# Optimization experiments

Hardware: AMD Instinct MI355X
Metric: run time of the kernel (lower is better)

The kernel has to match this reference:

```python
import jax, jax.numpy as jnp
import numpy as np

R = 32  # voxel resolution


def setup_inputs() -> dict:
    key = jax.random.key(0)
    k1, k2 = jax.random.split(key)
    B, C, N = 8, 64, 100000
    features = jax.random.normal(k1, (B, C, N), dtype=jnp.float32)
    coords = jax.random.uniform(k2, (B, 3, N), dtype=jnp.float32)  # unit cube [0,1]
    return {"features": features, "coords": coords}


def reference(features, coords):
    # features: [B, C, N], coords: [B, 3, N] in [0, 1]
    B, C, N = features.shape
    norm_coords = jnp.clip(coords * R, 0, R - 1)
    vox_coords = jnp.round(norm_coords).astype(jnp.int32)  # [B, 3, N]

    # flat voxel index per point: x*R^2 + y*R + z, offset per batch
    idx = vox_coords[:, 0] * R * R + vox_coords[:, 1] * R + vox_coords[:, 2]  # [B, N]
    flat_idx = (idx + jnp.arange(B, dtype=jnp.int32)[:, None] * (R ** 3)).reshape(-1)  # [B*N]

    feat = jnp.transpose(features, (0, 2, 1)).reshape(B * N, C)  # [B*N, C]
    sums = jax.ops.segment_sum(feat, flat_idx, num_segments=B * R ** 3)  # [B*R^3, C]
    cnt = jax.ops.segment_sum(jnp.ones((B * N,), features.dtype), flat_idx,
                              num_segments=B * R ** 3)  # [B*R^3]
    avg = sums / jnp.maximum(cnt, 1.0)[:, None]  # average; empty voxels stay 0

    vox_feat = jnp.transpose(avg.reshape(B, R ** 3, C), (0, 2, 1)).reshape(B, C, R, R, R)
    return vox_feat, vox_coords.astype(jnp.int64)
```

## Files before the change

kernel.cpp:

```cpp
#include <hip/hip_runtime.h>

#define RR 32
#define R3 32768
#define BATCH 8
#define CH 64
#define NPTS 100000
#define NPOINTS (BATCH * NPTS)
#define NVOX (BATCH * R3)
#define SCAN_BLOCKS (NVOX / 256)

typedef unsigned int uint32;

__device__ __forceinline__ uint32 f2bf(float f) {
    uint32 u = __float_as_uint(f);
    return (u + 0x7fffu + ((u >> 16) & 1u)) >> 16;
}
__device__ __forceinline__ float bf2f(uint32 h) {
    return __uint_as_float(h << 16);
}

__global__ __launch_bounds__(256) void phase1_count(
    const float* __restrict__ coords,
    uint32* __restrict__ vox,
    uint32* __restrict__ cnt,
    float* __restrict__ out2)
{
    int gid = blockIdx.x * blockDim.x + threadIdx.x;
    if (gid >= NPOINTS) return;
    int b = gid / NPTS;
    int n = gid - b * NPTS;

    const float* cb = coords + (size_t)b * 3 * NPTS + n;
    float fx = fminf(fmaxf(cb[0]        * 32.0f, 0.0f), 31.0f);
    float fy = fminf(fmaxf(cb[NPTS]     * 32.0f, 0.0f), 31.0f);
    float fz = fminf(fmaxf(cb[2 * NPTS] * 32.0f, 0.0f), 31.0f);
    int x = (int)rintf(fx);
    int y = (int)rintf(fy);
    int z = (int)rintf(fz);
    uint32 g = (uint32)(b * R3 + x * (RR * RR) + y * RR + z);

    float* o2 = out2 + (size_t)b * 3 * NPTS + n;
    o2[0]        = (float)x;
    o2[NPTS]     = (float)y;
    o2[2 * NPTS] = (float)z;

    vox[gid] = g;
    atomicAdd(&cnt[g], 1u);
}

__global__ __launch_bounds__(256) void scan_block_sums(
    const uint32* __restrict__ cnt, uint32* __restrict__ bsum)
{
    __shared__ uint32 s[256];
    int t = threadIdx.x;
    s[t] = cnt[blockIdx.x * 256 + t];
    __syncthreads();
    for (int off = 128; off > 0; off >>= 1) {
        if (t < off) s[t] += s[t + off];
        __syncthreads();
    }
    if (t == 0) bsum[blockIdx.x] = s[0];
}

__global__ __launch_bounds__(256) void scan_bsum(uint32* __restrict__ bsum)
{
    __shared__ uint32 s[256];
    int t = threadIdx.x;
    uint32 v0 = bsum[4 * t], v1 = bsum[4 * t + 1], v2 = bsum[4 * t + 2], v3 = bsum[4 * t + 3];
    uint32 tot = v0 + v1 + v2 + v3;
    s[t] = tot;
    __syncthreads();
    for (int off = 1; off < 256; off <<= 1) {
        uint32 x = (t >= off) ? s[t - off] : 0u;
        __syncthreads();
        s[t] += x;
        __syncthreads();
    }
    uint32 excl = s[t] - tot;
    bsum[4 * t]     = excl;
    bsum[4 * t + 1] = excl + v0;
    bsum[4 * t + 2] = excl + v0 + v1;
    bsum[4 * t + 3] = excl + v0 + v1 + v2;
}

__global__ __launch_bounds__(256) void scan_final(
    const uint32* __restrict__ cnt, const uint32* __restrict__ bsum,
    uint32* __restrict__ starts, uint32* __restrict__ cursor)
{
    __shared__ uint32 s[256];
    int t = threadIdx.x;
    int gid = blockIdx.x * 256 + t;
    uint32 v = cnt[gid];
    s[t] = v;
    __syncthreads();
    for (int off = 1; off < 256; off <<= 1) {
        uint32 x = (t >= off) ? s[t - off] : 0u;
        __syncthreads();
        s[t] += x;
        __syncthreads();
    }
    uint32 st = bsum[blockIdx.x] + s[t] - v;
    starts[gid] = st;
    cursor[gid] = st;
}

__global__ __launch_bounds__(256) void phase3_scatter(
    const float* __restrict__ feat,
    const uint32* __restrict__ vox,
    uint32* __restrict__ cursor,
    uint4* __restrict__ sorted)
{
    int gid = blockIdx.x * blockDim.x + threadIdx.x;
    if (gid >= NPOINTS) return;
    int b = gid / NPTS;
    int n = gid - b * NPTS;

    uint32 g = vox[gid];
    uint32 pos = atomicAdd(&cursor[g], 1u);

    const float* frow = feat + (size_t)b * CH * NPTS + n;
    uint4* dst = sorted + (size_t)pos * 8;
#pragma unroll
    for (int j = 0; j < 8; ++j) {
        uint4 w;
        float f0 = frow[(size_t)(8 * j + 0) * NPTS];
        float f1 = frow[(size_t)(8 * j + 1) * NPTS];
        float f2 = frow[(size_t)(8 * j + 2) * NPTS];
        float f3 = frow[(size_t)(8 * j + 3) * NPTS];
        float f4 = frow[(size_t)(8 * j + 4) * NPTS];
        float f5 = frow[(size_t)(8 * j + 5) * NPTS];
        float f6 = frow[(size_t)(8 * j + 6) * NPTS];
        float f7 = frow[(size_t)(8 * j + 7) * NPTS];
        w.x = f2bf(f0) | (f2bf(f1) << 16);
        w.y = f2bf(f2) | (f2bf(f3) << 16);
        w.z = f2bf(f4) | (f2bf(f5) << 16);
        w.w = f2bf(f6) | (f2bf(f7) << 16);
        dst[j] = w;
    }
}

__global__ __launch_bounds__(256) void phase4_reduce(
    const uint32* __restrict__ sorted,
    const uint32* __restrict__ starts,
    float* __restrict__ out1)
{
    __shared__ float tile[64][65];

    int gbase = blockIdx.x * 64;
    int tid = threadIdx.x;
    int wave = tid >> 6, lane = tid & 63;

    if (lane < 32) {
        for (int k = 0; k < 16; ++k) {
            int g = gbase + wave * 16 + k;
            uint32 s = starts[g];
            uint32 e = (g == NVOX - 1) ? (uint32)NPOINTS : starts[g + 1];
            float a0 = 0.0f, a1 = 0.0f;
            for (uint32 p = s; p < e; ++p) {
                uint32 w = sorted[(size_t)p * 32 + lane];
                a0 += bf2f(w & 0xffffu);
                a1 += bf2f(w >> 16);
            }
            uint32 c = e - s;
            float rcp = 1.0f / (float)(c > 1u ? c : 1u);
            int vloc = wave * 16 + k;
            tile[vloc][2 * lane]     = a0 * rcp;
            tile[vloc][2 * lane + 1] = a1 * rcp;
        }
    }
    __syncthreads();

    int b = gbase / R3;
    int v0 = gbase - b * R3;
    int vv = tid & 63;
    int c0 = tid >> 6;
    float* obase = out1 + (size_t)b * CH * R3 + v0 + vv;
#pragma unroll
    for (int jj = 0; jj < 16; ++jj) {
        int c = jj * 4 + c0;
        obase[(size_t)c * R3] = tile[vv][c];
    }
}

__global__ __launch_bounds__(256) void accum_direct(
    const float* __restrict__ feat, const float* __restrict__ coords,
    float* __restrict__ out1, uint32* __restrict__ cnt, float* __restrict__ out2)
{
    int gid = blockIdx.x * blockDim.x + threadIdx.x;
    if (gid >= NPOINTS) return;
    int b = gid / NPTS;
    int n = gid - b * NPTS;
    const float* cb = coords + (size_t)b * 3 * NPTS + n;
    float fx = fminf(fmaxf(cb[0]        * 32.0f, 0.0f), 31.0f);
    float fy = fminf(fmaxf(cb[NPTS]     * 32.0f, 0.0f), 31.0f);
    float fz = fminf(fmaxf(cb[2 * NPTS] * 32.0f, 0.0f), 31.0f);
    int x = (int)rintf(fx), y = (int)rintf(fy), z = (int)rintf(fz);
    int v = x * (RR * RR) + y * RR + z;
    float* o2 = out2 + (size_t)b * 3 * NPTS + n;
    o2[0] = (float)x; o2[NPTS] = (float)y; o2[2 * NPTS] = (float)z;
    atomicAdd(&cnt[b * R3 + v], 1u);
    float* obase = out1 + (size_t)(b * CH) * R3 + v;
    const float* frow = feat + (size_t)(b * CH) * NPTS + n;
#pragma unroll 8
    for (int c = 0; c < CH; ++c)
        unsafeAtomicAdd(&obase[(size_t)c * R3], frow[(size_t)c * NPTS]);
}

__global__ __launch_bounds__(256) void finalize_direct(
    float* __restrict__ out1, const uint32* __restrict__ cnt)
{
    size_t gid = (size_t)blockIdx.x * blockDim.x + threadIdx.x;
    size_t total = (size_t)BATCH * CH * R3;
    if (gid >= total) return;
    int v = (int)(gid & (R3 - 1));
    int b = (int)(gid / ((size_t)CH * R3));
    uint32 ct = cnt[b * R3 + v];
    out1[gid] = out1[gid] / (float)(ct > 1u ? ct : 1u);
}

extern "C" void kernel_launch(void* const* d_in, const int* in_sizes, int n_in,
                              void* d_out, int out_size, void* d_ws, size_t ws_size,
                              hipStream_t stream)
{
    const float* feat   = (const float*)d_in[0];
    const float* coords = (const float*)d_in[1];

    float* out1 = (float*)d_out;
    float* out2 = out1 + (size_t)BATCH * CH * R3;

    const size_t vox_off    = 0;
    const size_t vox_bytes  = (size_t)NPOINTS * 4;
    const size_t cnt_off    = vox_off + ((vox_bytes + 255) & ~255ull);
    const size_t cnt_bytes  = (size_t)NVOX * 4;
    const size_t starts_off = cnt_off + ((cnt_bytes + 255) & ~255ull);
    const size_t cursor_off = starts_off + ((cnt_bytes + 255) & ~255ull);
    const size_t bsum_off   = cursor_off + ((cnt_bytes + 255) & ~255ull);
    const size_t bsum_bytes = (size_t)SCAN_BLOCKS * 4;
    const size_t sort_off   = (bsum_off + bsum_bytes + 255) & ~255ull;
    const size_t sort_bytes = (size_t)NPOINTS * 128;
    const size_t need       = sort_off + sort_bytes;

    const int npt_blocks = (NPOINTS + 255) / 256;

    if (ws_size >= need) {
        char* ws = (char*)d_ws;
        uint32* vox    = (uint32*)(ws + vox_off);
        uint32* cnt    = (uint32*)(ws + cnt_off);
        uint32* starts = (uint32*)(ws + starts_off);
        uint32* cursor = (uint32*)(ws + cursor_off);
        uint32* bsum   = (uint32*)(ws + bsum_off);
        uint32* sorted = (uint32*)(ws + sort_off);

        hipMemsetAsync(cnt, 0, cnt_bytes, stream);
        phase1_count<<<npt_blocks, 256, 0, stream>>>(coords, vox, cnt, out2);
        scan_block_sums<<<SCAN_BLOCKS, 256, 0, stream>>>(cnt, bsum);
        scan_bsum<<<1, 256, 0, stream>>>(bsum);
        scan_final<<<SCAN_BLOCKS, 256, 0, stream>>>(cnt, bsum, starts, cursor);
        phase3_scatter<<<npt_blocks, 256, 0, stream>>>(feat, vox, cursor, (uint4*)sorted);
        phase4_reduce<<<NVOX / 64, 256, 0, stream>>>(sorted, starts, out1);
    } else {
        uint32* cnt = (uint32*)d_ws;
        hipMemsetAsync(out1, 0, (size_t)BATCH * CH * R3 * sizeof(float), stream);
        hipMemsetAsync(d_ws, 0, (size_t)NVOX * 4, stream);
        accum_direct<<<npt_blocks, 256, 0, stream>>>(feat, coords, out1, cnt, out2);
        size_t total = (size_t)BATCH * CH * R3;
        finalize_direct<<<(unsigned)((total + 255) / 256), 256, 0, stream>>>(out1, cnt);
    }
}
```

Before: 499.4 us.

## Replace counting-sort pipeline with per-(batch,channel) LDS atomic histogram accumulation

Drops the scan and sort-by-voxel pipeline (three scan kernels, a scatter into a bf16 sorted buffer, and a segmented reduce). Each block now owns one (batch, channel) pair and accumulates all 100k points into a 32768-float LDS array with shared-memory atomics, then divides by the counts and writes the output with coalesced float4 stores. Voxel indices are stored as 16-bit values to halve that traffic. This removes the bf16 rounding and the large sorted intermediate, but it uses 128KB of LDS per block, which limits occupancy, and it depends on LDS float atomics.

After: 522.9 us. +4.7%, slower.

```diff
diff --git a/kernel.cpp b/kernel.cpp
--- a/kernel.cpp
+++ b/kernel.cpp
@@ -7,21 +7,13 @@
 #define NPTS 100000
 #define NPOINTS (BATCH * NPTS)
 #define NVOX (BATCH * R3)
-#define SCAN_BLOCKS (NVOX / 256)
 
 typedef unsigned int uint32;
-
-__device__ __forceinline__ uint32 f2bf(float f) {
-    uint32 u = __float_as_uint(f);
-    return (u + 0x7fffu + ((u >> 16) & 1u)) >> 16;
-}
-__device__ __forceinline__ float bf2f(uint32 h) {
-    return __uint_as_float(h << 16);
-}
+typedef unsigned short uint16;
 
 __global__ __launch_bounds__(256) void phase1_count(
     const float* __restrict__ coords,
-    uint32* __restrict__ vox,
+    uint16* __restrict__ vox,
     uint32* __restrict__ cnt,
     float* __restrict__ out2)
 {
@@ -37,148 +29,63 @@
     int x = (int)rintf(fx);
     int y = (int)rintf(fy);
     int z = (int)rintf(fz);
-    uint32 g = (uint32)(b * R3 + x * (RR * RR) + y * RR + z);
+    int v = x * (RR * RR) + y * RR + z;
 
     float* o2 = out2 + (size_t)b * 3 * NPTS + n;
     o2[0]        = (float)x;
     o2[NPTS]     = (float)y;
     o2[2 * NPTS] = (float)z;
 
-    vox[gid] = g;
-    atomicAdd(&cnt[g], 1u);
+    vox[gid] = (uint16)v;
+    atomicAdd(&cnt[b * R3 + v], 1u);
 }
 
-__global__ __launch_bounds__(256) void scan_block_sums(
-    const uint32* __restrict__ cnt, uint32* __restrict__ bsum)
-{
-    __shared__ uint32 s[256];
-    int t = threadIdx.x;
-    s[t] = cnt[blockIdx.x * 256 + t];
-    __syncthreads();
-    for (int off = 128; off > 0; off >>= 1) {
-        if (t < off) s[t] += s[t + off];
-        __syncthreads();
-    }
-    if (t == 0) bsum[blockIdx.x] = s[0];
-}
-
-__global__ __launch_bounds__(256) void scan_bsum(uint32* __restrict__ bsum)
-{
-    __shared__ uint32 s[256];
-    int t = threadIdx.x;
-    uint32 v0 = bsum[4 * t], v1 = bsum[4 * t + 1], v2 = bsum[4 * t + 2], v3 = bsum[4 * t + 3];
-    uint32 tot = v0 + v1 + v2 + v3;
-    s[t] = tot;
-    __syncthreads();
-    for (int off = 1; off < 256; off <<= 1) {
-        uint32 x = (t >= off) ? s[t - off] : 0u;
-        __syncthreads();
-        s[t] += x;
-        __syncthreads();
-    }
-    uint32 excl = s[t] - tot;
-    bsum[4 * t]     = excl;
-    bsum[4 * t + 1] = excl + v0;
-    bsum[4 * t + 2] = excl + v0 + v1;
-    bsum[4 * t + 3] = excl + v0 + v1 + v2;
-}
-
-__global__ __launch_bounds__(256) void scan_final(
-    const uint32* __restrict__ cnt, const uint32* __restrict__ bsum,
-    uint32* __restrict__ starts, uint32* __restrict__ cursor)
-{
-    __shared__ uint32 s[256];
-    int t = threadIdx.x;
-    int gid = blockIdx.x * 256 + t;
-    uint32 v = cnt[gid];
-    s[t] = v;
-    __syncthreads();
-    for (int off = 1; off < 256; off <<= 1) {
-        uint32 x = (t >= off) ? s[t - off] : 0u;
-        __syncthreads();
-        s[t] += x;
-        __syncthreads();
-    }
-    uint32 st = bsum[blockIdx.x] + s[t] - v;
-    starts[gid] = st;
-    cursor[gid] = st;
-}
-
-__global__ __launch_bounds__(256) void phase3_scatter(
+__global__ __launch_bounds__(1024) void accum_lds(
     const float* __restrict__ feat,
-    const uint32* __restrict__ vox,
-    uint32* __restrict__ cursor,
-    uint4* __restrict__ sorted)
-{
-    int gid = blockIdx.x * blockDim.x + threadIdx.x;
-    if (gid >= NPOINTS) return;
-    int b = gid / NPTS;
-    int n = gid - b * NPTS;
-
-    uint32 g = vox[gid];
-    uint32 pos = atomicAdd(&cursor[g], 1u);
-
-    const float* frow = feat + (size_t)b * CH * NPTS + n;
-    uint4* dst = sorted + (size_t)pos * 8;
-#pragma unroll
-    for (int j = 0; j < 8; ++j) {
-        uint4 w;
-        float f0 = frow[(size_t)(8 * j + 0) * NPTS];
-        float f1 = frow[(size_t)(8 * j + 1) * NPTS];
-        float f2 = frow[(size_t)(8 * j + 2) * NPTS];
-        float f3 = frow[(size_t)(8 * j + 3) * NPTS];
-        float f4 = frow[(size_t)(8 * j + 4) * NPTS];
-        float f5 = frow[(size_t)(8 * j + 5) * NPTS];
-        float f6 = frow[(size_t)(8 * j + 6) * NPTS];
-        float f7 = frow[(size_t)(8 * j + 7) * NPTS];
-        w.x = f2bf(f0) | (f2bf(f1) << 16);
-        w.y = f2bf(f2) | (f2bf(f3) << 16);
-        w.z = f2bf(f4) | (f2bf(f5) << 16);
-        w.w = f2bf(f6) | (f2bf(f7) << 16);
-        dst[j] = w;
-    }
-}
-
-__global__ __launch_bounds__(256) void phase4_reduce(
-    const uint32* __restrict__ sorted,
-    const uint32* __restrict__ starts,
+    const uint16* __restrict__ vox,
+    const uint32* __restrict__ cnt,
     float* __restrict__ out1)
 {
-    __shared__ float tile[64][65];
+    extern __shared__ float acc[];
+    int b = blockIdx.x >> 6;
+    int c = blockIdx.x & 63;
+    int tid = threadIdx.x;
 
-    int gbase = blockIdx.x * 64;
-    int tid = threadIdx.x;
-    int wave = tid >> 6, lane = tid & 63;
+    float4* a4 = (float4*)acc;
+#pragma unroll
+    for (int i = 0; i < 8; ++i)
+        a4[i * 1024 + tid] = make_float4(0.f, 0.f, 0.f, 0.f);
+    __syncthreads();
 
-    if (lane < 32) {
-        for (int k = 0; k < 16; ++k) {
-            int g = gbase + wave * 16 + k;
-            uint32 s = starts[g];
-            uint32 e = (g == NVOX - 1) ? (uint32)NPOINTS : starts[g + 1];
-            float a0 = 0.0f, a1 = 0.0f;
-            for (uint32 p = s; p < e; ++p) {
-                uint32 w = sorted[(size_t)p * 32 + lane];
-                a0 += bf2f(w & 0xffffu);
-                a1 += bf2f(w >> 16);
-            }
-            uint32 c = e - s;
-            float rcp = 1.0f / (float)(c > 1u ? c : 1u);
-            int vloc = wave * 16 + k;
-            tile[vloc][2 * lane]     = a0 * rcp;
-            tile[vloc][2 * lane + 1] = a1 * rcp;
+    const float4*  f4 = (const float4*)(feat + ((size_t)b * CH + c) * NPTS);
+    const ushort4* v4 = (const ushort4*)(vox + (size_t)b * NPTS);
+    const int NQ = NPTS / 4;
+    for (int i = 0; i < 25; ++i) {
+        int idx = i * 1024 + tid;
+        if (idx < NQ) {
+            float4  f = f4[idx];
+            ushort4 v = v4[idx];
+            atomicAdd(&acc[v.x], f.x);
+            atomicAdd(&acc[v.y], f.y);
+            atomicAdd(&acc[v.z], f.z);
+            atomicAdd(&acc[v.w], f.w);
         }
     }
     __syncthreads();
 
-    int b = gbase / R3;
-    int v0 = gbase - b * R3;
-    int vv = tid & 63;
-    int c0 = tid >> 6;
-    float* obase = out1 + (size_t)b * CH * R3 + v0 + vv;
+    const uint4* c4 = (const uint4*)(cnt + (size_t)b * R3);
+    float4*      o4 = (float4*)(out1 + ((size_t)b * CH + c) * R3);
 #pragma unroll
-    for (int jj = 0; jj < 16; ++jj) {
-        int c = jj * 4 + c0;
-        obase[(size_t)c * R3] = tile[vv][c];
+    for (int i = 0; i < 8; ++i) {
+        int idx = i * 1024 + tid;
+        uint4  cc = c4[idx];
+        float4 s  = a4[idx];
+        float4 r;
+        r.x = s.x / (float)(cc.x > 1u ? cc.x : 1u);
+        r.y = s.y / (float)(cc.y > 1u ? cc.y : 1u);
+        r.z = s.z / (float)(cc.z > 1u ? cc.z : 1u);
+        r.w = s.w / (float)(cc.w > 1u ? cc.w : 1u);
+        o4[idx] = r;
     }
 }
 
@@ -228,36 +135,22 @@
     float* out1 = (float*)d_out;
     float* out2 = out1 + (size_t)BATCH * CH * R3;
 
-    const size_t vox_off    = 0;
-    const size_t vox_bytes  = (size_t)NPOINTS * 4;
-    const size_t cnt_off    = vox_off + ((vox_bytes + 255) & ~255ull);
-    const size_t cnt_bytes  = (size_t)NVOX * 4;
-    const size_t starts_off = cnt_off + ((cnt_bytes + 255) & ~255ull);
-    const size_t cursor_off = starts_off + ((cnt_bytes + 255) & ~255ull);
-    const size_t bsum_off   = cursor_off + ((cnt_bytes + 255) & ~255ull);
-    const size_t bsum_bytes = (size_t)SCAN_BLOCKS * 4;
-    const size_t sort_off   = (bsum_off + bsum_bytes + 255) & ~255ull;
-    const size_t sort_bytes = (size_t)NPOINTS * 128;
-    const size_t need       = sort_off + sort_bytes;
+    const size_t vox_off   = 0;
+    const size_t vox_bytes = (size_t)NPOINTS * 2;
+    const size_t cnt_off   = (vox_off + vox_bytes + 255) & ~255ull;
+    const size_t cnt_bytes = (size_t)NVOX * 4;
+    const size_t need      = cnt_off + cnt_bytes;
 
     const int npt_blocks = (NPOINTS + 255) / 256;
 
     if (ws_size >= need) {
         char* ws = (char*)d_ws;
-        uint32* vox    = (uint32*)(ws + vox_off);
-        uint32* cnt    = (uint32*)(ws + cnt_off);
-        uint32* starts = (uint32*)(ws + starts_off);
-        uint32* cursor = (uint32*)(ws + cursor_off);
-        uint32* bsum   = (uint32*)(ws + bsum_off);
-        uint32* sorted = (uint32*)(ws + sort_off);
+        uint16* vox = (uint16*)(ws + vox_off);
+        uint32* cnt = (uint32*)(ws + cnt_off);
 
         hipMemsetAsync(cnt, 0, cnt_bytes, stream);
         phase1_count<<<npt_blocks, 256, 0, stream>>>(coords, vox, cnt, out2);
-        scan_block_sums<<<SCAN_BLOCKS, 256, 0, stream>>>(cnt, bsum);
-        scan_bsum<<<1, 256, 0, stream>>>(bsum);
-        scan_final<<<SCAN_BLOCKS, 256, 0, stream>>>(cnt, bsum, starts, cursor);
-        phase3_scatter<<<npt_blocks, 256, 0, stream>>>(feat, vox, cursor, (uint4*)sorted);
-        phase4_reduce<<<NVOX / 64, 256, 0, stream>>>(sorted, starts, out1);
+        accum_lds<<<BATCH * CH, 1024, R3 * sizeof(float), stream>>>(feat, vox, cnt, out1);
     } else {
         uint32* cnt = (uint32*)d_ws;
         hipMemsetAsync(out1, 0, (size_t)BATCH * CH * R3 * sizeof(float), stream);
```

## Build voxel counts with per-block LDS histograms and split reduce across half-waves

Applied to the files above, without the earlier changes.

Replaces the global atomic count pass with 256 blocks that each build a 32K-bin shared-memory histogram for a slice of one batch's points. The partial histograms are written into the sorted buffer and summed in the first scan kernel, which removes the memset and the contended global atomics. The reduce kernel now has both halves of each wave process alternating points of a voxel and combines them with a shuffle, so all 64 lanes do work. The cost is a 128KB shared-memory histogram per block, which limits occupancy, plus 32 partial histograms per batch that must be read back in the scan.

New measurement: 445.0 us. 1.12x faster.

```diff
diff --git a/kernel.cpp b/kernel.cpp
--- a/kernel.cpp
+++ b/kernel.cpp
@@ -8,6 +8,8 @@
 #define NPOINTS (BATCH * NPTS)
 #define NVOX (BATCH * R3)
 #define SCAN_BLOCKS (NVOX / 256)
+#define HBLK 32
+#define PPB (NPTS / HBLK)
 
 typedef unsigned int uint32;
 
@@ -19,41 +21,65 @@
     return __uint_as_float(h << 16);
 }
 
-__global__ __launch_bounds__(256) void phase1_count(
+__global__ __launch_bounds__(256) void voxhist(
     const float* __restrict__ coords,
     uint32* __restrict__ vox,
-    uint32* __restrict__ cnt,
+    uint32* __restrict__ phist,
     float* __restrict__ out2)
 {
-    int gid = blockIdx.x * blockDim.x + threadIdx.x;
-    if (gid >= NPOINTS) return;
-    int b = gid / NPTS;
-    int n = gid - b * NPTS;
-
-    const float* cb = coords + (size_t)b * 3 * NPTS + n;
-    float fx = fminf(fmaxf(cb[0]        * 32.0f, 0.0f), 31.0f);
-    float fy = fminf(fmaxf(cb[NPTS]     * 32.0f, 0.0f), 31.0f);
-    float fz = fminf(fmaxf(cb[2 * NPTS] * 32.0f, 0.0f), 31.0f);
-    int x = (int)rintf(fx);
-    int y = (int)rintf(fy);
-    int z = (int)rintf(fz);
-    uint32 g = (uint32)(b * R3 + x * (RR * RR) + y * RR + z);
-
-    float* o2 = out2 + (size_t)b * 3 * NPTS + n;
-    o2[0]        = (float)x;
-    o2[NPTS]     = (float)y;
-    o2[2 * NPTS] = (float)z;
-
-    vox[gid] = g;
-    atomicAdd(&cnt[g], 1u);
-}
-
-__global__ __launch_bounds__(256) void scan_block_sums(
-    const uint32* __restrict__ cnt, uint32* __restrict__ bsum)
+    __shared__ uint32 hist[R3];
+
+    int b   = blockIdx.x >> 5;
+    int blk = blockIdx.x & 31;
+    int tid = threadIdx.x;
+
+    for (int i = tid; i < R3; i += 256) hist[i] = 0u;
+    __syncthreads();
+
+    int n0 = blk * PPB;
+    const float* cb = coords + (size_t)b * 3 * NPTS;
+    float*       o2 = out2   + (size_t)b * 3 * NPTS;
+
+    for (int i = tid; i < PPB; i += 256) {
+        int n = n0 + i;
+        float fx = fminf(fmaxf(cb[n]            * 32.0f, 0.0f), 31.0f);
+        float fy = fminf(fmaxf(cb[NPTS + n]     * 32.0f, 0.0f), 31.0f);
+        float fz = fminf(fmaxf(cb[2 * NPTS + n] * 32.0f, 0.0f), 31.0f);
+        int x = (int)rintf(fx);
+        int y = (int)rintf(fy);
+        int z = (int)rintf(fz);
+        int v = x * (RR * RR) + y * RR + z;
+
+        o2[n]            = (float)x;
+        o2[NPTS + n]     = (float)y;
+        o2[2 * NPTS + n] = (float)z;
+
+        vox[(size_t)b * NPTS + n] = (uint32)(b * R3 + v);
+        atomicAdd(&hist[v], 1u);
+    }
+    __syncthreads();
+
+    uint32* ph = phist + (size_t)(b * HBLK + blk) * R3;
+    for (int i = tid; i < R3; i += 256) ph[i] = hist[i];
+}
+
+__global__ __launch_bounds__(256) void scan_hist_sums(
+    const uint32* __restrict__ phist,
+    uint32* __restrict__ cnt, uint32* __restrict__ bsum)
 {
     __shared__ uint32 s[256];
     int t = threadIdx.x;
-    s[t] = cnt[blockIdx.x * 256 + t];
+    int gid = blockIdx.x * 256 + t;
+    int b = gid >> 15;
+    int v = gid & (R3 - 1);
+
+    const uint32* ph = phist + (size_t)b * HBLK * R3 + v;
+    uint32 c = 0;
+#pragma unroll
+    for (int k = 0; k < HBLK; ++k) c += ph[(size_t)k * R3];
+    cnt[gid] = c;
+
+    s[t] = c;
     __syncthreads();
     for (int off = 128; off > 0; off >>= 1) {
         if (t < off) s[t] += s[t + off];
@@ -148,24 +174,28 @@
 
     int gbase = blockIdx.x * 64;
     int tid = threadIdx.x;
-    int wave = tid >> 6, lane = tid & 63;
-
-    if (lane < 32) {
-        for (int k = 0; k < 16; ++k) {
-            int g = gbase + wave * 16 + k;
-            uint32 s = starts[g];
-            uint32 e = (g == NVOX - 1) ? (uint32)NPOINTS : starts[g + 1];
-            float a0 = 0.0f, a1 = 0.0f;
-            for (uint32 p = s; p < e; ++p) {
-                uint32 w = sorted[(size_t)p * 32 + lane];
-                a0 += bf2f(w & 0xffffu);
-                a1 += bf2f(w >> 16);
-            }
+    int w = tid >> 6, lane = tid & 63;
+    int half = lane >> 5;
+    int cp   = lane & 31;
+
+    for (int k = 0; k < 16; ++k) {
+        int g = gbase + w * 16 + k;
+        uint32 s = starts[g];
+        uint32 e = (g == NVOX - 1) ? (uint32)NPOINTS : starts[g + 1];
+        float a0 = 0.0f, a1 = 0.0f;
+        for (uint32 p = s + half; p < e; p += 2) {
+            uint32 d = sorted[(size_t)p * 32 + cp];
+            a0 += bf2f(d & 0xffffu);
+            a1 += bf2f(d >> 16);
+        }
+        a0 += __shfl_xor(a0, 32);
+        a1 += __shfl_xor(a1, 32);
+        if (half == 0) {
             uint32 c = e - s;
             float rcp = 1.0f / (float)(c > 1u ? c : 1u);
-            int vloc = wave * 16 + k;
-            tile[vloc][2 * lane]     = a0 * rcp;
-            tile[vloc][2 * lane + 1] = a1 * rcp;
+            int vloc = w * 16 + k;
+            tile[vloc][2 * cp]     = a0 * rcp;
+            tile[vloc][2 * cp + 1] = a1 * rcp;
         }
     }
     __syncthreads();
@@ -250,10 +280,10 @@
         uint32* cursor = (uint32*)(ws + cursor_off);
         uint32* bsum   = (uint32*)(ws + bsum_off);
         uint32* sorted = (uint32*)(ws + sort_off);
-
-        hipMemsetAsync(cnt, 0, cnt_bytes, stream);
-        phase1_count<<<npt_blocks, 256, 0, stream>>>(coords, vox, cnt, out2);
-        scan_block_sums<<<SCAN_BLOCKS, 256, 0, stream>>>(cnt, bsum);
+        uint32* phist  = sorted;
+
+        voxhist<<<BATCH * HBLK, 256, 0, stream>>>(coords, vox, phist, out2);
+        scan_hist_sums<<<SCAN_BLOCKS, 256, 0, stream>>>(phist, cnt, bsum);
         scan_bsum<<<1, 256, 0, stream>>>(bsum);
         scan_final<<<SCAN_BLOCKS, 256, 0, stream>>>(cnt, bsum, starts, cursor);
         phase3_scatter<<<npt_blocks, 256, 0, stream>>>(feat, vox, cursor, (uint4*)sorted);
```
